# Kernel tuning notes

Measured on AMD Instinct MI355X. Metric: run time of the kernel, lower is better.

Reference implementation:

```python
import jax, jax.numpy as jnp
import numpy as np

ENT_TYPE_SIZE = 9
INNER_DIM = 64
NEG_INF = 1e12


def _rope_interleaved(x, cos_pos, sin_pos):
    # x: (B, S, H, D); rotate interleaved pairs: (x0,x1)->(x0*c - x1*s, x1*c + x0*s)
    x2 = jnp.stack([-x[..., 1::2], x[..., ::2]], axis=-1).reshape(x.shape)
    return x * cos_pos + x2 * sin_pos


def setup_inputs() -> dict:
    key = jax.random.key(0)
    k1, k2 = jax.random.split(key)
    B, S, H = 16, 512, 768
    out_dim = ENT_TYPE_SIZE * INNER_DIM * 2  # 1152
    last_hidden_state = jax.random.normal(k1, (B, S, H), dtype=jnp.float32)
    attention_mask = jnp.ones((B, S), dtype=jnp.float32)
    W_dense = jax.random.normal(k2, (H, out_dim), dtype=jnp.float32) * (1.0 / np.sqrt(H))
    b_dense = jnp.zeros((out_dim,), dtype=jnp.float32)
    return {
        "last_hidden_state": last_hidden_state,
        "attention_mask": attention_mask,
        "W_dense": W_dense,
        "b_dense": b_dense,
    }


def reference(last_hidden_state, attention_mask, W_dense, b_dense):
    B, S, H = last_hidden_state.shape
    ent, inner = ENT_TYPE_SIZE, INNER_DIM

    # dense projection then split into per-entity-type q/k vectors
    proj = last_hidden_state @ W_dense + b_dense            # (B, S, ent*2*inner)
    proj = proj.reshape(B, S, ent, 2 * inner)
    qw, kw = proj[..., :inner], proj[..., inner:]           # (B, S, ent, inner)

    # inline RoPE, interleaved sin/cos layout per sinusoidal_position_embedding
    pos = jnp.arange(S, dtype=jnp.float32)[:, None]         # (S, 1)
    idx = jnp.arange(inner // 2, dtype=jnp.float32)
    freqs = pos * jnp.power(10000.0, -2.0 * idx / inner)    # (S, inner/2)
    cos_pos = jnp.repeat(jnp.cos(freqs), 2, axis=-1)[None, :, None, :]  # (1,S,1,inner)
    sin_pos = jnp.repeat(jnp.sin(freqs), 2, axis=-1)[None, :, None, :]
    qw = _rope_interleaved(qw, cos_pos, sin_pos)
    kw = _rope_interleaved(kw, cos_pos, sin_pos)

    # pairwise span scores
    logits = jnp.einsum('bmhd,bnhd->bhmn', qw, kw)          # (B, ent, S, S)

    # padding mask on key positions (canonical GlobalPointer masking)
    pad = attention_mask[:, None, None, :]                  # (B,1,1,S)
    logits = logits * pad - (1.0 - pad) * NEG_INF

    # strict lower triangle masked out (only spans with start <= end)
    tril = jnp.tril(jnp.ones((S, S), dtype=logits.dtype), -1)
    logits = logits - tril * NEG_INF

    return logits / (inner ** 0.5)
```

## Files before the change

kernel.cpp:

```cpp
#include <hip/hip_runtime.h>
#include <hip/hip_bf16.h>
#include <cstdint>

typedef __bf16 bf8 __attribute__((ext_vector_type(8)));
typedef __bf16 bf4 __attribute__((ext_vector_type(4)));
typedef float  f4  __attribute__((ext_vector_type(4)));

typedef const void __attribute__((address_space(1)))* as1_cvp;
typedef void       __attribute__((address_space(3)))* as3_vp;

#define NEG_INF_F 1000000000000.0f

__device__ __forceinline__ void lds_load16(const __bf16* g, __bf16* l) {
    __builtin_amdgcn_global_load_lds((as1_cvp)g, (as3_vp)l, 16, 0, 0);
}

__device__ __forceinline__ void gemm_tile_core(
    const __bf16* __restrict__ Atile, const __bf16* __restrict__ Btile,
    int lda, int ldb, int Ktot,
    __bf16* sA, __bf16* sB, f4 acc[4][4])
{
    const int t    = threadIdx.x;
    const int wave = t >> 6;
    const int lane = t & 63;
    const int quad = lane >> 4;
    const int m16  = lane & 15;
    const int wm   = (wave >> 1) * 64;
    const int wn   = (wave & 1) * 64;

    for (int k0 = 0; k0 < Ktot; k0 += 32) {
        __syncthreads();
#pragma unroll
        for (int i = 0; i < 2; ++i) {
            const int f   = i * 256 + t;
            const int row = f >> 2;
            const int ch  = (f & 3) * 8;
            lds_load16(Atile + (size_t)row * lda + k0 + ch,
                       sA + (i * 256 + wave * 64) * 8);
            lds_load16(Btile + (size_t)row * ldb + k0 + ch,
                       sB + (i * 256 + wave * 64) * 8);
        }
        __syncthreads();

        bf8 af[4], bfr[4];
#pragma unroll
        for (int mi = 0; mi < 4; ++mi)
            af[mi] = *(const bf8*)(sA + (wm + mi * 16 + m16) * 32 + quad * 8);
#pragma unroll
        for (int ni = 0; ni < 4; ++ni)
            bfr[ni] = *(const bf8*)(sB + (wn + ni * 16 + m16) * 32 + quad * 8);
#pragma unroll
        for (int mi = 0; mi < 4; ++mi)
#pragma unroll
            for (int ni = 0; ni < 4; ++ni)
                acc[mi][ni] = __builtin_amdgcn_mfma_f32_16x16x32_bf16(
                    af[mi], bfr[ni], acc[mi][ni], 0, 0, 0);
    }
}

__global__ __launch_bounds__(256) void cast_a_kernel(
    const float* __restrict__ in, __bf16* __restrict__ out, int n4)
{
    int idx = blockIdx.x * 256 + threadIdx.x;
    if (idx < n4) {
        const float4 v = reinterpret_cast<const float4*>(in)[idx];
        bf4 o = { (__bf16)v.x, (__bf16)v.y, (__bf16)v.z, (__bf16)v.w };
        reinterpret_cast<bf4*>(out)[idx] = o;
    }
}

__global__ __launch_bounds__(256) void transpose_w_kernel(
    const float* __restrict__ W, __bf16* __restrict__ Wt)
{
    __shared__ __bf16 tile[32][33];
    const int n0 = blockIdx.x * 32;
    const int k0 = blockIdx.y * 32;
    const int tx = threadIdx.x & 31;
    const int ty = threadIdx.x >> 5;
#pragma unroll
    for (int r = 0; r < 32; r += 8)
        tile[ty + r][tx] = (__bf16)W[(size_t)(k0 + ty + r) * 1152 + n0 + tx];
    __syncthreads();
#pragma unroll
    for (int r = 0; r < 32; r += 8)
        Wt[(size_t)(n0 + ty + r) * 768 + k0 + tx] = tile[tx][ty + r];
}

__global__ __launch_bounds__(256) void proj_rope_kernel(
    const __bf16* __restrict__ A,
    const __bf16* __restrict__ Wt,
    const float*  __restrict__ bias,
    __bf16* __restrict__ qbuf, __bf16* __restrict__ kbuf)
{
    __shared__ __bf16 sA[128 * 32];
    __shared__ __bf16 sB[128 * 32];
    f4 acc[4][4] = {};

    const int rowTile = blockIdx.y * 128;
    const int colTile = blockIdx.x * 128;
    gemm_tile_core(A + (size_t)rowTile * 768, Wt + (size_t)colTile * 768,
                   768, 768, 768, sA, sB, acc);

    const int t = threadIdx.x, wave = t >> 6, lane = t & 63;
    const int quad = lane >> 4, m16 = lane & 15;
    const int wm = (wave >> 1) * 64, wn = (wave & 1) * 64;

#pragma unroll
    for (int ni = 0; ni < 4; ++ni) {
        const int gc = colTile + wn + ni * 16 + m16;
        const float bv = bias[gc];
        const int e  = gc >> 7;
        const int d  = gc & 63;
        const int qk = (gc >> 6) & 1;
        const float theta = exp2f((float)(d >> 1) * -0.4152410118609203f);
        const float sgn = (d & 1) ? 1.0f : -1.0f;
        __bf16* dst = qk ? kbuf : qbuf;
#pragma unroll
        for (int mi = 0; mi < 4; ++mi) {
#pragma unroll
            for (int r = 0; r < 4; ++r) {
                const int gm = rowTile + wm + mi * 16 + quad * 4 + r;
                const int bb = gm >> 9;
                const int s  = gm & 511;
                float v = acc[mi][ni][r] + bv;
                float p = __shfl_xor(v, 1);
                float sn, cs;
                __sincosf((float)s * theta, &sn, &cs);
                float o = v * cs + sgn * p * sn;
                dst[(size_t)(((bb * 9 + e) * 512 + s)) * 64 + d] = (__bf16)o;
            }
        }
    }
}

__global__ __launch_bounds__(256, 3) void logits_kernel(
    const __bf16* __restrict__ qbuf, const __bf16* __restrict__ kbuf,
    const float* __restrict__ amask, float* __restrict__ out)
{
    const int t    = threadIdx.x;
    const int wave = t >> 6;
    const int lane = t & 63;
    const int quad = lane >> 4;
    const int m16  = lane & 15;
    const int wm   = (wave >> 1) * 64;
    const int ncol = (wave & 1) * 256;

    const int be = blockIdx.y;
    const int b  = be / 9;
    const int rowTile = blockIdx.x * 128;

    const __bf16* Qg = qbuf + (size_t)be * 512 * 64 + (size_t)(rowTile + wm) * 64;
    const __bf16* Kg = kbuf + (size_t)be * 512 * 64;

    bf8 af[2][4];
#pragma unroll
    for (int kp = 0; kp < 2; ++kp)
#pragma unroll
        for (int mi = 0; mi < 4; ++mi)
            af[kp][mi] = *reinterpret_cast<const bf8*>(
                Qg + (mi * 16 + m16) * 64 + kp * 32 + quad * 8);

    const float* amr  = amask + b * 512;
    float*       outw = out + ((size_t)(be * 512 + rowTile + wm) << 9);

#pragma unroll 1
    for (int c = 0; c < 4; ++c) {
        const int n0 = ncol + c * 64;
        const __bf16* Kc = Kg + (size_t)n0 * 64;

        bf8 bfr[2][4];
#pragma unroll
        for (int kp = 0; kp < 2; ++kp)
#pragma unroll
            for (int ni = 0; ni < 4; ++ni)
                bfr[kp][ni] = *reinterpret_cast<const bf8*>(
                    Kc + (ni * 16 + m16) * 64 + kp * 32 + quad * 8);

        f4 acc[4][4] = {};
#pragma unroll
        for (int kp = 0; kp < 2; ++kp)
#pragma unroll
            for (int mi = 0; mi < 4; ++mi)
#pragma unroll
                for (int ni = 0; ni < 4; ++ni)
                    acc[mi][ni] = __builtin_amdgcn_mfma_f32_16x16x32_bf16(
                        bfr[kp][ni], af[kp][mi], acc[mi][ni], 0, 0, 0);

#pragma unroll
        for (int ni = 0; ni < 4; ++ni) {
            const int nq = n0 + ni * 16 + quad * 4;
            const float4 pv = *reinterpret_cast<const float4*>(amr + nq);
#pragma unroll
            for (int mi = 0; mi < 4; ++mi) {
                const int m = rowTile + wm + mi * 16 + m16;
                const f4 a = acc[mi][ni];
                float4 res;
                float* rp = &res.x;
                const float pp[4] = { pv.x, pv.y, pv.z, pv.w };
#pragma unroll
                for (int r = 0; r < 4; ++r) {
                    float v = a[r] * pp[r] - (1.0f - pp[r]) * NEG_INF_F;
                    if (nq + r < m) v -= NEG_INF_F;
                    rp[r] = v * 0.125f;
                }
                *reinterpret_cast<float4*>(
                    outw + (((size_t)(mi * 16 + m16)) << 9) + nq) = res;
            }
        }
    }
}

extern "C" void kernel_launch(void* const* d_in, const int* in_sizes, int n_in,
                              void* d_out, int out_size, void* d_ws, size_t ws_size,
                              hipStream_t stream) {
    const float* lhs   = (const float*)d_in[0];
    const float* amask = (const float*)d_in[1];
    const float* W     = (const float*)d_in[2];
    const float* bias  = (const float*)d_in[3];
    float* out = (float*)d_out;

    char* ws = (char*)d_ws;
    __bf16* Abf = (__bf16*)ws;
    __bf16* Wt  = (__bf16*)(ws + 12582912);
    __bf16* qb  = (__bf16*)(ws + 14352384);
    __bf16* kb  = (__bf16*)(ws + 23789568);

    cast_a_kernel<<<6144, 256, 0, stream>>>(lhs, Abf, 1572864);
    transpose_w_kernel<<<dim3(36, 24), 256, 0, stream>>>(W, Wt);
    proj_rope_kernel<<<dim3(9, 64), 256, 0, stream>>>(Abf, Wt, bias, qb, kb);
    logits_kernel<<<dim3(4, 144), 256, 0, stream>>>(qb, kb, amask, out);
}
```

Baseline: 237.1 us.

## Skip fully-masked lower-triangle tiles, vectorize RoPE epilogue, merge prep kernels

The logits kernel now skips the MFMA work and K loads for 64-column chunks lying entirely below the diagonal, and writes the constant masked value there directly. The projection GEMM swaps MFMA operands so each lane holds four consecutive output columns, which lets the RoPE pairs be rotated in-register and stored as bf4 vectors instead of using a shuffle and scalar stores. The cast and transpose prep kernels are merged into one launch. The masked-chunk fill still depends on the runtime attention mask, so the output stays correct for any mask.

```diff
diff --git a/kernel.cpp b/kernel.cpp
--- a/kernel.cpp
+++ b/kernel.cpp
@@ -15,7 +15,7 @@
     __builtin_amdgcn_global_load_lds((as1_cvp)g, (as3_vp)l, 16, 0, 0);
 }
 
-__device__ __forceinline__ void gemm_tile_core(
+__device__ __forceinline__ void gemm_tile_core_swapped(
     const __bf16* __restrict__ Atile, const __bf16* __restrict__ Btile,
     int lda, int ldb, int Ktot,
     __bf16* sA, __bf16* sB, f4 acc[4][4])
@@ -54,36 +54,36 @@
 #pragma unroll
             for (int ni = 0; ni < 4; ++ni)
                 acc[mi][ni] = __builtin_amdgcn_mfma_f32_16x16x32_bf16(
-                    af[mi], bfr[ni], acc[mi][ni], 0, 0, 0);
-    }
-}
-
-__global__ __launch_bounds__(256) void cast_a_kernel(
-    const float* __restrict__ in, __bf16* __restrict__ out, int n4)
-{
-    int idx = blockIdx.x * 256 + threadIdx.x;
-    if (idx < n4) {
-        const float4 v = reinterpret_cast<const float4*>(in)[idx];
+                    bfr[ni], af[mi], acc[mi][ni], 0, 0, 0);
+    }
+}
+
+__global__ __launch_bounds__(256) void prep_kernel(
+    const float* __restrict__ lhs, __bf16* __restrict__ Abf,
+    const float* __restrict__ W,   __bf16* __restrict__ Wt)
+{
+    __shared__ __bf16 tile[32][33];
+    const int t  = threadIdx.x;
+    int bx = blockIdx.x;
+    if (bx < 6144) {
+        const int idx = bx * 256 + t;
+        const float4 v = reinterpret_cast<const float4*>(lhs)[idx];
         bf4 o = { (__bf16)v.x, (__bf16)v.y, (__bf16)v.z, (__bf16)v.w };
-        reinterpret_cast<bf4*>(out)[idx] = o;
-    }
-}
-
-__global__ __launch_bounds__(256) void transpose_w_kernel(
-    const float* __restrict__ W, __bf16* __restrict__ Wt)
-{
-    __shared__ __bf16 tile[32][33];
-    const int n0 = blockIdx.x * 32;
-    const int k0 = blockIdx.y * 32;
-    const int tx = threadIdx.x & 31;
-    const int ty = threadIdx.x >> 5;
-#pragma unroll
-    for (int r = 0; r < 32; r += 8)
-        tile[ty + r][tx] = (__bf16)W[(size_t)(k0 + ty + r) * 1152 + n0 + tx];
-    __syncthreads();
-#pragma unroll
-    for (int r = 0; r < 32; r += 8)
-        Wt[(size_t)(n0 + ty + r) * 768 + k0 + tx] = tile[tx][ty + r];
+        reinterpret_cast<bf4*>(Abf)[idx] = o;
+    } else {
+        bx -= 6144;
+        const int n0 = (bx % 36) * 32;
+        const int k0 = (bx / 36) * 32;
+        const int tx = t & 31;
+        const int ty = t >> 5;
+#pragma unroll
+        for (int r = 0; r < 32; r += 8)
+            tile[ty + r][tx] = (__bf16)W[(size_t)(k0 + ty + r) * 1152 + n0 + tx];
+        __syncthreads();
+#pragma unroll
+        for (int r = 0; r < 32; r += 8)
+            Wt[(size_t)(n0 + ty + r) * 768 + k0 + tx] = tile[tx][ty + r];
+    }
 }
 
 __global__ __launch_bounds__(256) void proj_rope_kernel(
@@ -98,8 +98,8 @@
 
     const int rowTile = blockIdx.y * 128;
     const int colTile = blockIdx.x * 128;
-    gemm_tile_core(A + (size_t)rowTile * 768, Wt + (size_t)colTile * 768,
-                   768, 768, 768, sA, sB, acc);
+    gemm_tile_core_swapped(A + (size_t)rowTile * 768, Wt + (size_t)colTile * 768,
+                           768, 768, 768, sA, sB, acc);
 
     const int t = threadIdx.x, wave = t >> 6, lane = t & 63;
     const int quad = lane >> 4, m16 = lane & 15;
@@ -107,28 +107,33 @@
 
 #pragma unroll
     for (int ni = 0; ni < 4; ++ni) {
-        const int gc = colTile + wn + ni * 16 + m16;
-        const float bv = bias[gc];
-        const int e  = gc >> 7;
-        const int d  = gc & 63;
-        const int qk = (gc >> 6) & 1;
-        const float theta = exp2f((float)(d >> 1) * -0.4152410118609203f);
-        const float sgn = (d & 1) ? 1.0f : -1.0f;
-        __bf16* dst = qk ? kbuf : qbuf;
+        const int gc0 = colTile + wn + ni * 16 + quad * 4;
+        const int e   = gc0 >> 7;
+        const int d0  = gc0 & 63;
+        const int qk  = (gc0 >> 6) & 1;
+        const float4 bv = *reinterpret_cast<const float4*>(bias + gc0);
+        const float th0 = exp2f((float)(d0 >> 1)       * -0.4152410118609203f);
+        const float th1 = exp2f((float)((d0 >> 1) + 1) * -0.4152410118609203f);
+        __bf16* base = (qk ? kbuf : qbuf);
 #pragma unroll
         for (int mi = 0; mi < 4; ++mi) {
-#pragma unroll
-            for (int r = 0; r < 4; ++r) {
-                const int gm = rowTile + wm + mi * 16 + quad * 4 + r;
-                const int bb = gm >> 9;
-                const int s  = gm & 511;
-                float v = acc[mi][ni][r] + bv;
-                float p = __shfl_xor(v, 1);
-                float sn, cs;
-                __sincosf((float)s * theta, &sn, &cs);
-                float o = v * cs + sgn * p * sn;
-                dst[(size_t)(((bb * 9 + e) * 512 + s)) * 64 + d] = (__bf16)o;
-            }
+            const int gm = rowTile + wm + mi * 16 + m16;
+            const int bb = gm >> 9;
+            const int s  = gm & 511;
+            const float sf = (float)s;
+            float v0 = acc[mi][ni][0] + bv.x;
+            float v1 = acc[mi][ni][1] + bv.y;
+            float v2 = acc[mi][ni][2] + bv.z;
+            float v3 = acc[mi][ni][3] + bv.w;
+            float sn0, cs0, sn1, cs1;
+            __sincosf(sf * th0, &sn0, &cs0);
+            __sincosf(sf * th1, &sn1, &cs1);
+            bf4 o = { (__bf16)(v0 * cs0 - v1 * sn0),
+                      (__bf16)(v1 * cs0 + v0 * sn0),
+                      (__bf16)(v2 * cs1 - v3 * sn1),
+                      (__bf16)(v3 * cs1 + v2 * sn1) };
+            *reinterpret_cast<bf4*>(
+                base + ((size_t)((bb * 9 + e) * 512 + s)) * 64 + d0) = o;
         }
     }
 }
@@ -148,8 +153,12 @@
     const int be = blockIdx.y;
     const int b  = be / 9;
     const int rowTile = blockIdx.x * 128;
-
-    const __bf16* Qg = qbuf + (size_t)be * 512 * 64 + (size_t)(rowTile + wm) * 64;
+    const int rowbase = rowTile + wm;
+
+    int c0 = (rowbase - ncol) >> 6;
+    c0 = c0 < 0 ? 0 : (c0 > 4 ? 4 : c0);
+
+    const __bf16* Qg = qbuf + (size_t)be * 512 * 64 + (size_t)rowbase * 64;
     const __bf16* Kg = kbuf + (size_t)be * 512 * 64;
 
     bf8 af[2][4];
@@ -161,50 +170,67 @@
                 Qg + (mi * 16 + m16) * 64 + kp * 32 + quad * 8);
 
     const float* amr  = amask + b * 512;
-    float*       outw = out + ((size_t)(be * 512 + rowTile + wm) << 9);
-
-#pragma unroll 1
+    float*       outw = out + ((size_t)(be * 512 + rowbase) << 9);
+
+#pragma unroll
     for (int c = 0; c < 4; ++c) {
         const int n0 = ncol + c * 64;
-        const __bf16* Kc = Kg + (size_t)n0 * 64;
-
-        bf8 bfr[2][4];
-#pragma unroll
-        for (int kp = 0; kp < 2; ++kp)
-#pragma unroll
-            for (int ni = 0; ni < 4; ++ni)
-                bfr[kp][ni] = *reinterpret_cast<const bf8*>(
-                    Kc + (ni * 16 + m16) * 64 + kp * 32 + quad * 8);
-
-        f4 acc[4][4] = {};
-#pragma unroll
-        for (int kp = 0; kp < 2; ++kp)
-#pragma unroll
-            for (int mi = 0; mi < 4; ++mi)
+        if (c >= c0) {
+            const __bf16* Kc = Kg + (size_t)n0 * 64;
+            bf8 bfr[2][4];
+#pragma unroll
+            for (int kp = 0; kp < 2; ++kp)
 #pragma unroll
                 for (int ni = 0; ni < 4; ++ni)
-                    acc[mi][ni] = __builtin_amdgcn_mfma_f32_16x16x32_bf16(
-                        bfr[kp][ni], af[kp][mi], acc[mi][ni], 0, 0, 0);
-
-#pragma unroll
-        for (int ni = 0; ni < 4; ++ni) {
-            const int nq = n0 + ni * 16 + quad * 4;
-            const float4 pv = *reinterpret_cast<const float4*>(amr + nq);
-#pragma unroll
-            for (int mi = 0; mi < 4; ++mi) {
-                const int m = rowTile + wm + mi * 16 + m16;
-                const f4 a = acc[mi][ni];
+                    bfr[kp][ni] = *reinterpret_cast<const bf8*>(
+                        Kc + (ni * 16 + m16) * 64 + kp * 32 + quad * 8);
+
+            f4 acc[4][4] = {};
+#pragma unroll
+            for (int kp = 0; kp < 2; ++kp)
+#pragma unroll
+                for (int mi = 0; mi < 4; ++mi)
+#pragma unroll
+                    for (int ni = 0; ni < 4; ++ni)
+                        acc[mi][ni] = __builtin_amdgcn_mfma_f32_16x16x32_bf16(
+                            bfr[kp][ni], af[kp][mi], acc[mi][ni], 0, 0, 0);
+
+#pragma unroll
+            for (int ni = 0; ni < 4; ++ni) {
+                const int nq = n0 + ni * 16 + quad * 4;
+                const float4 pv = *reinterpret_cast<const float4*>(amr + nq);
+                const float pp[4] = { pv.x, pv.y, pv.z, pv.w };
+#pragma unroll
+                for (int mi = 0; mi < 4; ++mi) {
+                    const int m = rowbase + mi * 16 + m16;
+                    const f4 a = acc[mi][ni];
+                    float4 res;
+                    float* rp = &res.x;
+#pragma unroll
+                    for (int r = 0; r < 4; ++r) {
+                        float v = a[r] * pp[r] - (1.0f - pp[r]) * NEG_INF_F;
+                        if (nq + r < m) v -= NEG_INF_F;
+                        rp[r] = v * 0.125f;
+                    }
+                    *reinterpret_cast<float4*>(
+                        outw + (((size_t)(mi * 16 + m16)) << 9) + nq) = res;
+                }
+            }
+        } else {
+#pragma unroll
+            for (int ni = 0; ni < 4; ++ni) {
+                const int nq = n0 + ni * 16 + quad * 4;
+                const float4 pv = *reinterpret_cast<const float4*>(amr + nq);
+                const float pp[4] = { pv.x, pv.y, pv.z, pv.w };
                 float4 res;
                 float* rp = &res.x;
-                const float pp[4] = { pv.x, pv.y, pv.z, pv.w };
-#pragma unroll
-                for (int r = 0; r < 4; ++r) {
-                    float v = a[r] * pp[r] - (1.0f - pp[r]) * NEG_INF_F;
-                    if (nq + r < m) v -= NEG_INF_F;
-                    rp[r] = v * 0.125f;
-                }
-                *reinterpret_cast<float4*>(
-                    outw + (((size_t)(mi * 16 + m16)) << 9) + nq) = res;
+#pragma unroll
+                for (int r = 0; r < 4; ++r)
+                    rp[r] = (-(1.0f - pp[r]) * NEG_INF_F - NEG_INF_F) * 0.125f;
+#pragma unroll
+                for (int mi = 0; mi < 4; ++mi)
+                    *reinterpret_cast<float4*>(
+                        outw + (((size_t)(mi * 16 + m16)) << 9) + nq) = res;
             }
         }
     }
@@ -225,8 +251,7 @@
     __bf16* qb  = (__bf16*)(ws + 14352384);
     __bf16* kb  = (__bf16*)(ws + 23789568);
 
-    cast_a_kernel<<<6144, 256, 0, stream>>>(lhs, Abf, 1572864);
-    transpose_w_kernel<<<dim3(36, 24), 256, 0, stream>>>(W, Wt);
+    prep_kernel<<<7008, 256, 0, stream>>>(lhs, Abf, W, Wt);
     proj_rope_kernel<<<dim3(9, 64), 256, 0, stream>>>(Abf, Wt, bias, qb, kb);
     logits_kernel<<<dim3(4, 144), 256, 0, stream>>>(qb, kb, amask, out);
 }
```

New measurement: 226.9 us. 1.05x faster.
